# Kernel optimization log

Measured on AMD Instinct MI355X. Metric: run time of the kernel, lower is better.

## Reference

```python
import math
import jax, jax.numpy as jnp
import numpy as np

B, LQ, LK, D, H = 4, 2048, 2048, 512, 8  # dim_Q=dim_K=dim_V=D, num_heads=H


def _layernorm(x, g, b, eps=1e-5):
    mu = jnp.mean(x, axis=-1, keepdims=True)
    var = jnp.var(x, axis=-1, keepdims=True)
    return (x - mu) * jax.lax.rsqrt(var + eps) * g + b


def setup_inputs() -> dict:
    key = jax.random.key(0)
    ks = jax.random.split(key, 16)
    s = 1.0 / math.sqrt(D)
    return {
        "Q": jax.random.normal(ks[0], (B, LQ, D), jnp.float32),
        "K": jax.random.normal(ks[1], (B, LK, D), jnp.float32),
        "pad_mask": jax.random.randint(ks[2], (B, LK), 0, 2, jnp.int32),
        "Wq": jax.random.normal(ks[3], (D, D), jnp.float32) * s,
        "bq": jnp.zeros((D,), jnp.float32),
        "Wk": jax.random.normal(ks[4], (D, D), jnp.float32) * s,
        "bk": jnp.zeros((D,), jnp.float32),
        "Wv": jax.random.normal(ks[5], (D, D), jnp.float32) * s,
        "bv": jnp.zeros((D,), jnp.float32),
        "Wo": jax.random.normal(ks[6], (D, D), jnp.float32) * s,
        "bo": jnp.zeros((D,), jnp.float32),
        "g0": jnp.ones((D,), jnp.float32),
        "b0": jnp.zeros((D,), jnp.float32),
        "g1": jnp.ones((D,), jnp.float32),
        "b1": jnp.zeros((D,), jnp.float32),
    }


def reference(Q, K, pad_mask, Wq, bq, Wk, bk, Wv, bv, Wo, bo, g0, b0, g1, b1):
    d = D // H  # head dim (torch: split(dim_split, 2) then cat along batch)
    Qh = (Q @ Wq + bq).reshape(B, LQ, H, d)
    Kh = (K @ Wk + bk).reshape(B, LK, H, d)
    Vh = (K @ Wv + bv).reshape(B, LK, H, d)
    # NOTE: original scales by sqrt(dim_V), not sqrt(head_dim)
    score = jnp.einsum('bqhd,bkhd->bhqk', Qh, Kh) / np.float32(math.sqrt(D))
    m = pad_mask[:, None, None, :].astype(score.dtype)  # (B,1,1,Lk)
    score = jnp.where(m == 0, jnp.float32(-1e12), score)
    A = jax.nn.softmax(score, axis=-1) * m  # post-softmax mask multiply (faithful)
    O = jnp.einsum('bhqk,bkhd->bqhd', A, Vh).reshape(B, LQ, D)
    O = Q + O
    O = _layernorm(O, g0, b0)
    O = O + jax.nn.relu(O @ Wo + bo)
    O = _layernorm(O, g1, b1)
    return O
```

## Files before the change

kernel.cpp:

```cpp
#include <hip/hip_runtime.h>
#include <math.h>

#define NB   4
#define SLQ  2048
#define SLK  2048
#define DIM  512
#define NH   8
#define HD   64
#define NROWS (NB * SLQ)
#define NT   (SLK / 64)

typedef __attribute__((ext_vector_type(8)))  __bf16 bf16x8;
typedef __attribute__((ext_vector_type(4)))  __bf16 bf16x4;
typedef __attribute__((ext_vector_type(2)))  __bf16 bf16x2;
typedef __attribute__((ext_vector_type(4)))  float  f32x4;
typedef __attribute__((ext_vector_type(16))) float  f32x16;
typedef __attribute__((ext_vector_type(4)))  unsigned int u32x4;

typedef const __attribute__((address_space(1))) void* as1_cptr;
typedef __attribute__((address_space(3))) void*       as3_ptr;
__device__ __forceinline__ void async_ld16(const void* g, void* s) {
    __builtin_amdgcn_global_load_lds((as1_cptr)g, (as3_ptr)s, 16, 0, 0);
}

__global__ __launch_bounds__(256)
void transpose_w_kernel(const float* __restrict__ Wq, const float* __restrict__ Wk,
                        const float* __restrict__ Wv, const float* __restrict__ Wo,
                        const int* __restrict__ maskp,
                        __bf16* __restrict__ Wt, float* __restrict__ msentg) {
    const int m = blockIdx.z;
    const int t = threadIdx.x;
    if (m == 4) {
        const int idx = (blockIdx.y * 16 + blockIdx.x) * 256 + t;
        if (idx < NB * SLK) msentg[idx] = maskp[idx] ? 0.f : -1e30f;
        return;
    }
    __shared__ float Ls[32][33];
    const float* W = (m == 0) ? Wq : (m == 1) ? Wk : (m == 2) ? Wv : Wo;
    const int k0 = blockIdx.y * 32, n0 = blockIdx.x * 32;
    const int r  = t >> 3, c = (t & 7) * 4;

    const float4 v = *reinterpret_cast<const float4*>(&W[(size_t)(k0 + r) * DIM + n0 + c]);
    Ls[r][c + 0] = v.x; Ls[r][c + 1] = v.y; Ls[r][c + 2] = v.z; Ls[r][c + 3] = v.w;
    __syncthreads();

    const int n = t >> 3, k = (t & 7) * 4;
    bf16x4 o;
    o[0] = (__bf16)Ls[k + 0][n];
    o[1] = (__bf16)Ls[k + 1][n];
    o[2] = (__bf16)Ls[k + 2][n];
    o[3] = (__bf16)Ls[k + 3][n];
    *reinterpret_cast<bf16x4*>(&Wt[(size_t)(512 * m + n0 + n) * DIM + k0 + k]) = o;
}

__global__ __launch_bounds__(256)
void proj_mfma_kernel(const float* __restrict__ Qp, const float* __restrict__ Kp,
                      const __bf16* __restrict__ Wt,
                      const float* __restrict__ bq, const float* __restrict__ bk,
                      const float* __restrict__ bv,
                      __bf16* __restrict__ Qh, __bf16* __restrict__ Kh,
                      __bf16* __restrict__ VhT) {
    __shared__ __bf16 As[128][72];
    __shared__ __bf16 Bs[128][64];

    const int bx   = blockIdx.x;
    const int mode = bx >> 2;
    const int cb   = bx & 3;
    const float*  A    = (mode == 0) ? Qp : Kp;
    const __bf16* Bt   = Wt + (size_t)(mode * 512) * DIM;
    const float*  bias = ((mode == 0) ? bq : (mode == 1) ? bk : bv) + cb * 128;
    const int col0 = cb * 128;

    const int t  = threadIdx.x;
    const int w  = t >> 6, l = t & 63, lg = l >> 4, lc = l & 15;
    const int wr = w >> 1, wc = w & 1;
    const int row0 = blockIdx.y * 128;

    f32x4 acc[4][4];
    #pragma unroll
    for (int mi = 0; mi < 4; ++mi)
        #pragma unroll
        for (int nj = 0; nj < 4; ++nj) acc[mi][nj] = f32x4{0.f, 0.f, 0.f, 0.f};

    const int sr   = t >> 3, sc = (t & 7) * 8;
    const int srow = l >> 3;
    const int schk = (l & 7) ^ srow;
    const int x7   = lc & 7;

    for (int k0 = 0; k0 < DIM; k0 += 64) {
        __syncthreads();
        #pragma unroll
        for (int i = 0; i < 4; ++i) {
            const int r = i * 32 + sr;
            const float4 a0 = *reinterpret_cast<const float4*>(
                &A[(size_t)(row0 + r) * DIM + k0 + sc]);
            const float4 a1 = *reinterpret_cast<const float4*>(
                &A[(size_t)(row0 + r) * DIM + k0 + sc + 4]);
            bf16x8 hv;
            hv[0] = (__bf16)a0.x; hv[1] = (__bf16)a0.y;
            hv[2] = (__bf16)a0.z; hv[3] = (__bf16)a0.w;
            hv[4] = (__bf16)a1.x; hv[5] = (__bf16)a1.y;
            hv[6] = (__bf16)a1.z; hv[7] = (__bf16)a1.w;
            *reinterpret_cast<bf16x8*>(&As[r][sc]) = hv;
        }
        #pragma unroll
        for (int i = 0; i < 4; ++i) {
            const int rb = w * 32 + i * 8;
            async_ld16(Bt + (size_t)(col0 + rb + srow) * DIM + k0 + schk * 8,
                       &Bs[rb][0]);
        }
        __syncthreads();

        #pragma unroll
        for (int ks = 0; ks < 2; ++ks) {
            bf16x8 af[4], bfv[4];
            #pragma unroll
            for (int mi = 0; mi < 4; ++mi)
                af[mi] = *reinterpret_cast<const bf16x8*>(
                    &As[wr * 64 + mi * 16 + lc][ks * 32 + lg * 8]);
            #pragma unroll
            for (int nj = 0; nj < 4; ++nj) {
                const int rowb = wc * 64 + nj * 16 + lc;
                bfv[nj] = *reinterpret_cast<const bf16x8*>(
                    &Bs[rowb][(((ks * 4 + lg) ^ x7) << 3)]);
            }
            #pragma unroll
            for (int mi = 0; mi < 4; ++mi)
                #pragma unroll
                for (int nj = 0; nj < 4; ++nj)
                    acc[mi][nj] = __builtin_amdgcn_mfma_f32_16x16x32_bf16(
                        af[mi], bfv[nj], acc[mi][nj], 0, 0, 0);
        }
    }

    #pragma unroll
    for (int mi = 0; mi < 4; ++mi) {
        #pragma unroll
        for (int nj = 0; nj < 4; ++nj) {
            const int cl  = wc * 64 + nj * 16 + lc;
            const float bb = bias[cl];
            if (mode == 2) {
                const int dcol = col0 + cl;
                const int hh = dcol >> 6, dd = dcol & 63;
                const int row = row0 + wr * 64 + mi * 16 + lg * 4;
                const int bi  = row >> 11, key = row & 2047;
                bf16x4 pk;
                #pragma unroll
                for (int r = 0; r < 4; ++r) pk[r] = (__bf16)(acc[mi][nj][r] + bb);
                *reinterpret_cast<bf16x4*>(
                    &VhT[((size_t)(bi * NH + hh) * HD + dd) * SLK + key]) = pk;
            } else {
                __bf16* out = (mode == 0) ? Qh : Kh;
                #pragma unroll
                for (int r = 0; r < 4; ++r) {
                    const int row = row0 + wr * 64 + mi * 16 + lg * 4 + r;
                    out[(size_t)row * DIM + col0 + cl] = (__bf16)(acc[mi][nj][r] + bb);
                }
            }
        }
    }
}

__global__ __launch_bounds__(256)
void ffn_mfma_kernel(const __bf16* __restrict__ A, const __bf16* __restrict__ Bt,
                     const float* __restrict__ bias, __bf16* __restrict__ outv) {
    __shared__ __bf16 As[128][72];
    __shared__ __bf16 Bs[64][72];

    const int t  = threadIdx.x;
    const int w  = t >> 6, l = t & 63, lg = l >> 4, lc = l & 15;
    const int wr = w >> 1, wc = w & 1;
    const int row0 = blockIdx.y * 128, col0 = blockIdx.x * 64;

    f32x4 acc[4][2];
    #pragma unroll
    for (int mi = 0; mi < 4; ++mi)
        #pragma unroll
        for (int nj = 0; nj < 2; ++nj) acc[mi][nj] = f32x4{0.f, 0.f, 0.f, 0.f};

    const int sr = t >> 3, sc = (t & 7) * 8;

    for (int k0 = 0; k0 < DIM; k0 += 64) {
        __syncthreads();
        #pragma unroll
        for (int i = 0; i < 4; ++i) {
            const int r = i * 32 + sr;
            *reinterpret_cast<bf16x8*>(&As[r][sc]) =
                *reinterpret_cast<const bf16x8*>(&A[(size_t)(row0 + r) * DIM + k0 + sc]);
        }
        #pragma unroll
        for (int i = 0; i < 2; ++i) {
            const int n = i * 32 + sr;
            *reinterpret_cast<bf16x8*>(&Bs[n][sc]) =
                *reinterpret_cast<const bf16x8*>(&Bt[(size_t)(col0 + n) * DIM + k0 + sc]);
        }
        __syncthreads();

        #pragma unroll
        for (int ks = 0; ks < 2; ++ks) {
            bf16x8 af[4], bfv[2];
            #pragma unroll
            for (int mi = 0; mi < 4; ++mi)
                af[mi] = *reinterpret_cast<const bf16x8*>(
                    &As[wr * 64 + mi * 16 + lc][ks * 32 + lg * 8]);
            #pragma unroll
            for (int nj = 0; nj < 2; ++nj)
                bfv[nj] = *reinterpret_cast<const bf16x8*>(
                    &Bs[wc * 32 + nj * 16 + lc][ks * 32 + lg * 8]);
            #pragma unroll
            for (int mi = 0; mi < 4; ++mi)
                #pragma unroll
                for (int nj = 0; nj < 2; ++nj)
                    acc[mi][nj] = __builtin_amdgcn_mfma_f32_16x16x32_bf16(
                        af[mi], bfv[nj], acc[mi][nj], 0, 0, 0);
        }
    }

    #pragma unroll
    for (int mi = 0; mi < 4; ++mi) {
        #pragma unroll
        for (int nj = 0; nj < 2; ++nj) {
            const int cl  = wc * 32 + nj * 16 + lc;
            const int col = col0 + cl;
            #pragma unroll
            for (int r = 0; r < 4; ++r) {
                const int row = row0 + wr * 64 + mi * 16 + lg * 4 + r;
                const float vv = acc[mi][nj][r] + bias[col];
                outv[(size_t)row * DIM + col] =
                    (__bf16)((float)A[(size_t)row * DIM + col] + fmaxf(vv, 0.f));
            }
        }
    }
}

__global__ __launch_bounds__(256)
void attn_mfma_kernel(const __bf16* __restrict__ Qh, const __bf16* __restrict__ Kh,
                      const __bf16* __restrict__ VhT, const float* __restrict__ msentg,
                      __bf16* __restrict__ Oa) {
    const int pos  = blockIdx.x;
    const int orig = (pos & 7) * 64 + (pos >> 3);
    const int qb = orig & 15;
    const int h  = (orig >> 4) & 7;
    const int b  = orig >> 7;

    const int tid = threadIdx.x;
    const int w   = tid >> 6;
    const int l   = tid & 63;
    const int ql  = l & 31;
    const int hi  = l >> 5;
    const int x7  = ql & 7;

    __shared__ __bf16 Ks[3][64][64];
    __shared__ __bf16 Vt[3][64][64];
    __shared__ float  msent[SLK];
    __shared__ float  linv[4][32];

    {
        const float* mb = msentg + b * SLK;
        #pragma unroll
        for (int i = 0; i < 2; ++i) {
            const int idx = (i * 256 + tid) * 4;
            *reinterpret_cast<f32x4*>(&msent[idx]) =
                *reinterpret_cast<const f32x4*>(&mb[idx]);
        }
    }

    const int q0 = qb * 128 + w * 32;
    bf16x8 qf[4];
    {
        const __bf16* qrow = Qh + (size_t)(b * SLQ + q0 + ql) * DIM + h * HD + hi * 8;
        #pragma unroll
        for (int c = 0; c < 4; ++c)
            qf[c] = *reinterpret_cast<const bf16x8*>(qrow + c * 16);
    }

    const __bf16* kbase = Kh  + (size_t)b * SLK * DIM + h * HD;
    const __bf16* vbase = VhT + (size_t)(b * NH + h) * HD * SLK;

    const int srow = l >> 3;
    const int schk = (l & 7) ^ srow;

    auto STAGE = [&](int nb_, int k0_) {
        #pragma unroll
        for (int i = 0; i < 2; ++i) {
            const int rb = w * 16 + i * 8;
            async_ld16(kbase + (size_t)(k0_ + rb + srow) * DIM + schk * 8,
                       &Ks[nb_][rb][0]);
            async_ld16(vbase + (size_t)(rb + srow) * SLK + k0_ + schk * 8,
                       &Vt[nb_][rb][0]);
        }
    };

    f32x16 oacc[2];
    #pragma unroll
    for (int i = 0; i < 16; ++i) { oacc[0][i] = 0.f; oacc[1][i] = 0.f; }
    float l_part = 0.f;
    const float scale2 = 0.06377551f;

    STAGE(0, 0);
    STAGE(1, 64);
    asm volatile("s_waitcnt lgkmcnt(0)" ::: "memory");

    int rd = 0;
    for (int t = 0; t < NT; ++t) {
        if (t == NT - 1) asm volatile("s_waitcnt vmcnt(0)" ::: "memory");
        else             asm volatile("s_waitcnt vmcnt(4)" ::: "memory");
        __builtin_amdgcn_s_barrier();

        if (t + 2 < NT) {
            const int st = (rd + 2 >= 3) ? rd - 1 : rd + 2;
            STAGE(st, (t + 2) * 64);
        }

        const int k0 = t * 64;
        const __bf16* KsC = &Ks[rd][0][0];
        const __bf16* VtC = &Vt[rd][0][0];

        f32x16 sacc[2];
        #pragma unroll
        for (int i = 0; i < 16; ++i) { sacc[0][i] = 0.f; sacc[1][i] = 0.f; }
        __builtin_amdgcn_s_setprio(1);
        #pragma unroll
        for (int kb = 0; kb < 2; ++kb) {
            #pragma unroll
            for (int c = 0; c < 4; ++c) {
                const bf16x8 kf = *reinterpret_cast<const bf16x8*>(
                    &KsC[(kb * 32 + ql) * 64 + (((2 * c + hi) ^ x7) << 3)]);
                sacc[kb] = __builtin_amdgcn_mfma_f32_32x32x16_bf16(
                    kf, qf[c], sacc[kb], 0, 0, 0);
            }
        }
        __builtin_amdgcn_s_setprio(0);

        unsigned int P2[2][8];
        #pragma unroll
        for (int kb = 0; kb < 2; ++kb) {
            #pragma unroll
            for (int m = 0; m < 4; ++m) {
                const f32x4 tm = *reinterpret_cast<const f32x4*>(
                    &msent[k0 + kb * 32 + 8 * m + 4 * hi]);
                float p[4];
                #pragma unroll
                for (int j = 0; j < 4; ++j) {
                    p[j] = __builtin_amdgcn_exp2f(
                        fmaf(sacc[kb][4 * m + j], scale2, tm[j]));
                    l_part += p[j];
                }
                bf16x2 w0, w1;
                w0[0] = (__bf16)p[0]; w0[1] = (__bf16)p[1];
                w1[0] = (__bf16)p[2]; w1[1] = (__bf16)p[3];
                P2[kb][2 * m]     = __builtin_bit_cast(unsigned int, w0);
                P2[kb][2 * m + 1] = __builtin_bit_cast(unsigned int, w1);
            }
        }

        #pragma unroll
        for (int kb = 0; kb < 2; ++kb) {
            #pragma unroll
            for (int cc = 0; cc < 2; ++cc) {
                asm volatile("v_permlane32_swap_b32 %0, %1"
                             : "+v"(P2[kb][4 * cc + 0]), "+v"(P2[kb][4 * cc + 2]));
                asm volatile("v_permlane32_swap_b32 %0, %1"
                             : "+v"(P2[kb][4 * cc + 1]), "+v"(P2[kb][4 * cc + 3]));
            }
        }
        bf16x8 pfrag[4];
        #pragma unroll
        for (int c = 0; c < 4; ++c) {
            const int kb = c >> 1, cc = c & 1;
            u32x4 fw;
            fw.x = P2[kb][4 * cc + 0]; fw.y = P2[kb][4 * cc + 1];
            fw.z = P2[kb][4 * cc + 2]; fw.w = P2[kb][4 * cc + 3];
            pfrag[c] = __builtin_bit_cast(bf16x8, fw);
        }

        __builtin_amdgcn_s_setprio(1);
        #pragma unroll
        for (int db = 0; db < 2; ++db) {
            #pragma unroll
            for (int c = 0; c < 4; ++c) {
                const bf16x8 vf = *reinterpret_cast<const bf16x8*>(
                    &VtC[(db * 32 + ql) * 64 + (((2 * c + hi) ^ x7) << 3)]);
                oacc[db] = __builtin_amdgcn_mfma_f32_32x32x16_bf16(
                    pfrag[c], vf, oacc[db], 0, 0, 0);
            }
        }
        __builtin_amdgcn_s_setprio(0);

        rd = (rd == 2) ? 0 : rd + 1;
    }

    const float lsum = l_part + __shfl_xor(l_part, 32, 64);
    if (hi == 0) linv[w][ql] = (lsum > 0.f) ? 1.f / lsum : 0.f;
    #pragma unroll
    for (int db = 0; db < 2; ++db) {
        #pragma unroll
        for (int m = 0; m < 4; ++m) {
            const f32x4 iv = *reinterpret_cast<const f32x4*>(&linv[w][8 * m + 4 * hi]);
            #pragma unroll
            for (int j = 0; j < 4; ++j) {
                const int qr = 8 * m + 4 * hi + j;
                Oa[(size_t)(b * SLQ + q0 + qr) * DIM + h * HD + db * 32 + ql] =
                    (__bf16)(oacc[db][4 * m + j] * iv[j]);
            }
        }
    }
}

__device__ __forceinline__ float wave_sum(float v) {
    #pragma unroll
    for (int off = 32; off > 0; off >>= 1) v += __shfl_xor(v, off, 64);
    return v;
}

__global__ __launch_bounds__(256)
void ln1_kernel(const __bf16* X, const float* Y,
                const float* g, const float* bta, __bf16* out) {
    const int w    = threadIdx.x >> 6;
    const int lane = threadIdx.x & 63;
    const int row  = blockIdx.x * 4 + w;
    const size_t base = (size_t)row * DIM + lane * 8;

    const bf16x8 xv = *reinterpret_cast<const bf16x8*>(&X[base]);
    const float4 y0 = *reinterpret_cast<const float4*>(&Y[base]);
    const float4 y1 = *reinterpret_cast<const float4*>(&Y[base + 4]);
    float v[8];
    v[0] = (float)xv[0] + y0.x; v[1] = (float)xv[1] + y0.y;
    v[2] = (float)xv[2] + y0.z; v[3] = (float)xv[3] + y0.w;
    v[4] = (float)xv[4] + y1.x; v[5] = (float)xv[5] + y1.y;
    v[6] = (float)xv[6] + y1.z; v[7] = (float)xv[7] + y1.w;

    float s = 0.f, ss = 0.f;
    #pragma unroll
    for (int i = 0; i < 8; ++i) { s += v[i]; ss += v[i] * v[i]; }
    s  = wave_sum(s);
    ss = wave_sum(ss);
    const float mean = s * (1.f / DIM);
    const float var  = ss * (1.f / DIM) - mean * mean;
    const float rstd = rsqrtf(var + 1e-5f);

    const float4 g0 = *reinterpret_cast<const float4*>(&g[lane * 8]);
    const float4 g1 = *reinterpret_cast<const float4*>(&g[lane * 8 + 4]);
    const float4 b0 = *reinterpret_cast<const float4*>(&bta[lane * 8]);
    const float4 b1 = *reinterpret_cast<const float4*>(&bta[lane * 8 + 4]);
    float gg[8] = {g0.x, g0.y, g0.z, g0.w, g1.x, g1.y, g1.z, g1.w};
    float bb[8] = {b0.x, b0.y, b0.z, b0.w, b1.x, b1.y, b1.z, b1.w};

    bf16x8 o;
    #pragma unroll
    for (int i = 0; i < 8; ++i)
        o[i] = (__bf16)((v[i] - mean) * rstd * gg[i] + bb[i]);
    *reinterpret_cast<bf16x8*>(&out[base]) = o;
}

__global__ __launch_bounds__(256)
void ln2_kernel(const __bf16* X, const float* g, const float* bta, float* out) {
    const int w    = threadIdx.x >> 6;
    const int lane = threadIdx.x & 63;
    const int row  = blockIdx.x * 4 + w;
    const size_t base = (size_t)row * DIM + lane * 8;

    const bf16x8 xv = *reinterpret_cast<const bf16x8*>(&X[base]);
    float v[8];
    #pragma unroll
    for (int i = 0; i < 8; ++i) v[i] = (float)xv[i];

    float s = 0.f, ss = 0.f;
    #pragma unroll
    for (int i = 0; i < 8; ++i) { s += v[i]; ss += v[i] * v[i]; }
    s  = wave_sum(s);
    ss = wave_sum(ss);
    const float mean = s * (1.f / DIM);
    const float var  = ss * (1.f / DIM) - mean * mean;
    const float rstd = rsqrtf(var + 1e-5f);

    const float4 g0 = *reinterpret_cast<const float4*>(&g[lane * 8]);
    const float4 g1 = *reinterpret_cast<const float4*>(&g[lane * 8 + 4]);
    const float4 b0 = *reinterpret_cast<const float4*>(&bta[lane * 8]);
    const float4 b1 = *reinterpret_cast<const float4*>(&bta[lane * 8 + 4]);
    float gg[8] = {g0.x, g0.y, g0.z, g0.w, g1.x, g1.y, g1.z, g1.w};
    float bb[8] = {b0.x, b0.y, b0.z, b0.w, b1.x, b1.y, b1.z, b1.w};

    float4 o0, o1;
    o0.x = (v[0] - mean) * rstd * gg[0] + bb[0];
    o0.y = (v[1] - mean) * rstd * gg[1] + bb[1];
    o0.z = (v[2] - mean) * rstd * gg[2] + bb[2];
    o0.w = (v[3] - mean) * rstd * gg[3] + bb[3];
    o1.x = (v[4] - mean) * rstd * gg[4] + bb[4];
    o1.y = (v[5] - mean) * rstd * gg[5] + bb[5];
    o1.z = (v[6] - mean) * rstd * gg[6] + bb[6];
    o1.w = (v[7] - mean) * rstd * gg[7] + bb[7];
    *reinterpret_cast<float4*>(&out[base])     = o0;
    *reinterpret_cast<float4*>(&out[base + 4]) = o1;
}

extern "C" void kernel_launch(void* const* d_in, const int* in_sizes, int n_in,
                              void* d_out, int out_size, void* d_ws, size_t ws_size,
                              hipStream_t stream) {
    const float* Q     = (const float*)d_in[0];
    const float* K     = (const float*)d_in[1];
    const int*   maskp = (const int*)  d_in[2];
    const float* Wq    = (const float*)d_in[3];
    const float* bq    = (const float*)d_in[4];
    const float* Wk    = (const float*)d_in[5];
    const float* bk    = (const float*)d_in[6];
    const float* Wv    = (const float*)d_in[7];
    const float* bv    = (const float*)d_in[8];
    const float* Wo    = (const float*)d_in[9];
    const float* bo    = (const float*)d_in[10];
    const float* g0    = (const float*)d_in[11];
    const float* b0    = (const float*)d_in[12];
    const float* g1    = (const float*)d_in[13];
    const float* b1    = (const float*)d_in[14];

    float* out = (float*)d_out;
    char*  ws  = (char*)d_ws;
    __bf16* Qh     = (__bf16*)ws;
    __bf16* Kh     = (__bf16*)(ws + (8u  << 20));
    __bf16* VhT    = (__bf16*)(ws + (16u << 20));
    __bf16* Wt     = (__bf16*)(ws + (24u << 20));
    __bf16* Oa     = (__bf16*)(ws + (26u << 20));
    __bf16* H1     = (__bf16*)(ws + (34u << 20));
    float*  msentg = (float*)(ws + (42u << 20));
    __bf16* R2     = (__bf16*)ws;

    transpose_w_kernel<<<dim3(16, 16, 5), 256, 0, stream>>>(
        Wq, Wk, Wv, Wo, maskp, Wt, msentg);

    proj_mfma_kernel<<<dim3(12, 64), 256, 0, stream>>>(
        Q, K, Wt, bq, bk, bv, Qh, Kh, VhT);

    attn_mfma_kernel<<<dim3(512), 256, 0, stream>>>(Qh, Kh, VhT, msentg, Oa);

    ln1_kernel<<<NROWS / 4, 256, 0, stream>>>(Oa, Q, g0, b0, H1);

    ffn_mfma_kernel<<<dim3(8, 64), 256, 0, stream>>>(
        H1, Wt + (size_t)1536 * DIM, bo, R2);

    ln2_kernel<<<NROWS / 4, 256, 0, stream>>>(R2, g1, b1, out);
}
```

Baseline: 138.7 us.

## Double-buffer projection GEMM with register-prefetched A and async B staging

Restructures the QKV projection GEMM main loop into a two-stage software pipeline. The next fp32 A tile is held in registers and the next B tile is staged asynchronously into a second LDS buffer while MFMAs run on the current one, with explicit vmcnt waits and one barrier per iteration. The A tile in LDS now uses an XOR swizzle in place of padding, and the bias values are hoisted into registers. The aim is to hide global-load latency behind compute, at the cost of more LDS and registers plus hand-counted waitcnt logic that could break if load counts change.

Result: no change. 139.4 us (+0.5%).

```diff
diff --git a/kernel.cpp b/kernel.cpp
--- a/kernel.cpp
+++ b/kernel.cpp
@@ -60,15 +60,15 @@
                       const float* __restrict__ bv,
                       __bf16* __restrict__ Qh, __bf16* __restrict__ Kh,
                       __bf16* __restrict__ VhT) {
-    __shared__ __bf16 As[128][72];
-    __shared__ __bf16 Bs[128][64];
+    __shared__ __bf16 As[2][128][64];
+    __shared__ __bf16 Bs[2][128][64];
 
     const int bx   = blockIdx.x;
     const int mode = bx >> 2;
     const int cb   = bx & 3;
-    const float*  A    = (mode == 0) ? Qp : Kp;
-    const __bf16* Bt   = Wt + (size_t)(mode * 512) * DIM;
-    const float*  bias = ((mode == 0) ? bq : (mode == 1) ? bk : bv) + cb * 128;
+    const float*  Ag = (mode == 0) ? Qp : Kp;
+    const __bf16* Bt = Wt + (size_t)(mode * 512) * DIM;
+    const float*  biasp = ((mode == 0) ? bq : (mode == 1) ? bk : bv) + cb * 128;
     const int col0 = cb * 128;
 
     const int t  = threadIdx.x;
@@ -76,40 +76,55 @@
     const int wr = w >> 1, wc = w & 1;
     const int row0 = blockIdx.y * 128;
 
-    f32x4 acc[4][4];
-    #pragma unroll
-    for (int mi = 0; mi < 4; ++mi)
-        #pragma unroll
-        for (int nj = 0; nj < 4; ++nj) acc[mi][nj] = f32x4{0.f, 0.f, 0.f, 0.f};
-
-    const int sr   = t >> 3, sc = (t & 7) * 8;
+    float biasr[4];
+    #pragma unroll
+    for (int nj = 0; nj < 4; ++nj) biasr[nj] = biasp[wc * 64 + nj * 16 + lc];
+    asm volatile("s_waitcnt vmcnt(0)" ::: "memory");
+
+    const int sr   = t >> 3;
+    const int sc8  = t & 7;
+    const int swA  = (sc8 ^ (sr & 7)) * 8;
     const int srow = l >> 3;
     const int schk = (l & 7) ^ srow;
     const int x7   = lc & 7;
 
-    for (int k0 = 0; k0 < DIM; k0 += 64) {
-        __syncthreads();
-        #pragma unroll
-        for (int i = 0; i < 4; ++i) {
-            const int r = i * 32 + sr;
-            const float4 a0 = *reinterpret_cast<const float4*>(
-                &A[(size_t)(row0 + r) * DIM + k0 + sc]);
-            const float4 a1 = *reinterpret_cast<const float4*>(
-                &A[(size_t)(row0 + r) * DIM + k0 + sc + 4]);
-            bf16x8 hv;
-            hv[0] = (__bf16)a0.x; hv[1] = (__bf16)a0.y;
-            hv[2] = (__bf16)a0.z; hv[3] = (__bf16)a0.w;
-            hv[4] = (__bf16)a1.x; hv[5] = (__bf16)a1.y;
-            hv[6] = (__bf16)a1.z; hv[7] = (__bf16)a1.w;
-            *reinterpret_cast<bf16x8*>(&As[r][sc]) = hv;
-        }
-        #pragma unroll
-        for (int i = 0; i < 4; ++i) {
-            const int rb = w * 32 + i * 8;
-            async_ld16(Bt + (size_t)(col0 + rb + srow) * DIM + k0 + schk * 8,
-                       &Bs[rb][0]);
-        }
-        __syncthreads();
+    f32x4 acc[4][4];
+    #pragma unroll
+    for (int mi = 0; mi < 4; ++mi)
+        #pragma unroll
+        for (int nj = 0; nj < 4; ++nj) acc[mi][nj] = f32x4{0.f, 0.f, 0.f, 0.f};
+
+    float4 areg[4][2];
+
+#define PROJ_CF asm volatile("" ::: "memory")
+#define PROJ_ISSUE_A(k0_) { _Pragma("unroll") for (int i = 0; i < 4; ++i) {    \
+        const float* ap = Ag + (size_t)(row0 + i * 32 + sr) * DIM + (k0_) + sc8 * 8; \
+        areg[i][0] = *reinterpret_cast<const float4*>(ap);                     \
+        areg[i][1] = *reinterpret_cast<const float4*>(ap + 4); } PROJ_CF; }
+#define PROJ_CVT(nb_) { _Pragma("unroll") for (int i = 0; i < 4; ++i) {        \
+        bf16x8 hv;                                                             \
+        hv[0] = (__bf16)areg[i][0].x; hv[1] = (__bf16)areg[i][0].y;            \
+        hv[2] = (__bf16)areg[i][0].z; hv[3] = (__bf16)areg[i][0].w;            \
+        hv[4] = (__bf16)areg[i][1].x; hv[5] = (__bf16)areg[i][1].y;            \
+        hv[6] = (__bf16)areg[i][1].z; hv[7] = (__bf16)areg[i][1].w;            \
+        *reinterpret_cast<bf16x8*>(&As[nb_][i * 32 + sr][swA]) = hv; } }
+#define PROJ_STAGE_B(nb_, k0_) { _Pragma("unroll") for (int i = 0; i < 4; ++i) { \
+        const int rb = w * 32 + i * 8;                                         \
+        async_ld16(Bt + (size_t)(col0 + rb + srow) * DIM + (k0_) + schk * 8,   \
+                   &Bs[nb_][rb][0]); } PROJ_CF; }
+
+    PROJ_ISSUE_A(0);
+    asm volatile("s_waitcnt vmcnt(0)" ::: "memory");
+    PROJ_CVT(0);
+    PROJ_STAGE_B(0, 0);
+    PROJ_ISSUE_A(64);
+    asm volatile("s_waitcnt vmcnt(8)" ::: "memory");
+    asm volatile("s_waitcnt lgkmcnt(0)" ::: "memory");
+    __builtin_amdgcn_s_barrier();
+
+    for (int kt = 0; kt < 8; ++kt) {
+        const int cur = kt & 1;
+        if (kt + 1 < 8) PROJ_STAGE_B((kt + 1) & 1, (kt + 1) * 64);
 
         #pragma unroll
         for (int ks = 0; ks < 2; ++ks) {
@@ -117,13 +132,11 @@
             #pragma unroll
             for (int mi = 0; mi < 4; ++mi)
                 af[mi] = *reinterpret_cast<const bf16x8*>(
-                    &As[wr * 64 + mi * 16 + lc][ks * 32 + lg * 8]);
-            #pragma unroll
-            for (int nj = 0; nj < 4; ++nj) {
-                const int rowb = wc * 64 + nj * 16 + lc;
+                    &As[cur][wr * 64 + mi * 16 + lc][((ks * 4 + lg) ^ x7) << 3]);
+            #pragma unroll
+            for (int nj = 0; nj < 4; ++nj)
                 bfv[nj] = *reinterpret_cast<const bf16x8*>(
-                    &Bs[rowb][(((ks * 4 + lg) ^ x7) << 3)]);
-            }
+                    &Bs[cur][wc * 64 + nj * 16 + lc][((ks * 4 + lg) ^ x7) << 3]);
             #pragma unroll
             for (int mi = 0; mi < 4; ++mi)
                 #pragma unroll
@@ -131,6 +144,19 @@
                     acc[mi][nj] = __builtin_amdgcn_mfma_f32_16x16x32_bf16(
                         af[mi], bfv[nj], acc[mi][nj], 0, 0, 0);
         }
+
+        if (kt + 1 < 8) {
+            asm volatile("s_waitcnt vmcnt(4)" ::: "memory");
+            PROJ_CVT((kt + 1) & 1);
+            if (kt + 2 < 8) {
+                PROJ_ISSUE_A((kt + 2) * 64);
+                asm volatile("s_waitcnt vmcnt(8)" ::: "memory");
+            } else {
+                asm volatile("s_waitcnt vmcnt(0)" ::: "memory");
+            }
+            asm volatile("s_waitcnt lgkmcnt(0)" ::: "memory");
+            __builtin_amdgcn_s_barrier();
+        }
     }
 
     #pragma unroll
@@ -138,7 +164,7 @@
         #pragma unroll
         for (int nj = 0; nj < 4; ++nj) {
             const int cl  = wc * 64 + nj * 16 + lc;
-            const float bb = bias[cl];
+            const float bb = biasr[nj];
             if (mode == 2) {
                 const int dcol = col0 + cl;
                 const int hh = dcol >> 6, dd = dcol & 63;
```
